# Kernel optimization log

Hardware: AMD Instinct MI355X
Metric: run time of the kernel (lower is better)

Reference implementation:

```python
import jax, jax.numpy as jnp
import numpy as np

T = 8192        # timesteps
IN = 512        # input_size
H = 1024        # hidden_layer_size
OUT = 256       # output_size
STEP = 0.25     # ODE solver step_size
NSUB = 4        # euler substeps per unit time interval (t spacing = 1)


def setup_inputs() -> dict:
    key = jax.random.key(0)
    ks = jax.random.split(key, 16)
    def lin(k, out_d, in_d):
        kw, kb = jax.random.split(k)
        W = jax.random.normal(kw, (out_d, in_d), jnp.float32) / np.sqrt(in_d).astype(np.float32)
        b = jax.random.normal(kb, (out_d, 1), jnp.float32) * 0.01
        return W, b
    W_in, b_in = lin(ks[0], H, IN)      # linear_in
    W_h, b_h = lin(ks[1], H, H)         # linear_hidden
    W_h2, b_h2 = lin(ks[2], H, H)       # linear_hidden2
    W_f1, b_f1 = lin(ks[3], H, H)       # ode_func.linear
    W_f2, b_f2 = lin(ks[4], H, H)       # ode_func.linear2
    W_dec, b_dec = lin(ks[5], OUT, H)   # decoder
    x = jax.random.normal(ks[6], (T, IN, 1), jnp.float32)
    t = jnp.arange(T, dtype=jnp.float32)
    return dict(t=t, x=x, W_in=W_in, b_in=b_in, W_h=W_h, b_h=b_h,
                W_h2=W_h2, b_h2=b_h2, W_f1=W_f1, b_f1=b_f1,
                W_f2=W_f2, b_f2=b_f2, W_dec=W_dec, b_dec=b_dec)


def reference(t, x, W_in, b_in, W_h, b_h, W_h2, b_h2, W_f1, b_f1, W_f2, b_f2, W_dec, b_dec):
    # ODE_Func: f(h) = W_f2 @ tanh(W_f1 @ h + b_f1) + b_f2   (autonomous; t unused)
    def ode_f(h):
        return W_f2 @ jnp.tanh(W_f1 @ h + b_f1) + b_f2

    dts = (t[1:] - t[:-1]) / NSUB  # (T-1,) euler substep sizes (fixed-grid euler)

    def step(h, inp):
        x_i, dt = inp
        # odeint(ode_func, h, t[i-1:i+1], method='euler', step_size=STEP)
        for _ in range(NSUB):
            h = h + dt * ode_f(h)
        # RNN cell update
        pre = W_in @ x_i + b_in + W_h @ h + b_h          # (H,1)
        h_new = jnp.tanh(W_h2 @ jnp.tanh(pre) + b_h2)    # (H,1)
        return h_new, None

    h0 = jnp.zeros((W_h.shape[0], 1), x.dtype)
    # original loop skips i == 0 entirely (h stays zeros there)
    h_T, _ = jax.lax.scan(step, h0, (x[1:], dts))
    return W_dec @ h_T + b_dec  # (OUT, 1)
```

## Files before the change

kernel.cpp:

```cpp
#include <hip/hip_runtime.h>
#include <math.h>


#define TSTEPS 8192
#define INP    512
#define HDIM   1024
#define OUTD   256
#define NWG    64
#define BLK    256
#define NREP   8

typedef unsigned long long u64;
typedef unsigned int u32;

__device__ __forceinline__ u64 aload(u64* p) {
    return __hip_atomic_load(p, __ATOMIC_RELAXED, __HIP_MEMORY_SCOPE_AGENT);
}
__device__ __forceinline__ void astore(u64* p, u64 v) {
    __hip_atomic_store(p, v, __ATOMIC_RELAXED, __HIP_MEMORY_SCOPE_AGENT);
}
__device__ __forceinline__ u64 pack(u32 tag, float f) {
    return ((u64)tag << 32) | (u64)__float_as_uint(f);
}

__global__ __launch_bounds__(256)
void mm1024(const float* __restrict__ A, const float* __restrict__ B,
            float* __restrict__ C) {
    __shared__ float As[64][17];
    __shared__ float Bs[16][65];
    const int tid = threadIdx.x;
    const int tx = tid & 15, ty = tid >> 4;
    const int r0 = blockIdx.y * 64, c0 = blockIdx.x * 64;
    float acc[4][4] = {};
    for (int k0 = 0; k0 < HDIM; k0 += 16) {
        const int ar = tid >> 2, ac = (tid & 3) * 4;
        const float4 av = *reinterpret_cast<const float4*>(
            A + (size_t)(r0 + ar) * HDIM + k0 + ac);
        As[ar][ac] = av.x; As[ar][ac + 1] = av.y;
        As[ar][ac + 2] = av.z; As[ar][ac + 3] = av.w;
        const int br = tid >> 4, bc = (tid & 15) * 4;
        const float4 bv = *reinterpret_cast<const float4*>(
            B + (size_t)(k0 + br) * HDIM + c0 + bc);
        Bs[br][bc] = bv.x; Bs[br][bc + 1] = bv.y;
        Bs[br][bc + 2] = bv.z; Bs[br][bc + 3] = bv.w;
        __syncthreads();
        #pragma unroll
        for (int kk = 0; kk < 16; ++kk) {
            float a[4], b[4];
            #pragma unroll
            for (int i2 = 0; i2 < 4; ++i2) a[i2] = As[ty * 4 + i2][kk];
            #pragma unroll
            for (int j2 = 0; j2 < 4; ++j2) b[j2] = Bs[kk][tx * 4 + j2];
            #pragma unroll
            for (int i2 = 0; i2 < 4; ++i2)
                #pragma unroll
                for (int j2 = 0; j2 < 4; ++j2)
                    acc[i2][j2] = fmaf(a[i2], b[j2], acc[i2][j2]);
        }
        __syncthreads();
    }
    #pragma unroll
    for (int i2 = 0; i2 < 4; ++i2)
        #pragma unroll
        for (int j2 = 0; j2 < 4; ++j2)
            C[(size_t)(r0 + ty * 4 + i2) * HDIM + c0 + tx * 4 + j2] = acc[i2][j2];
}

__global__ __launch_bounds__(BLK, 1)
void ode_rnn_persistent(
    const float* __restrict__ t,    const float* __restrict__ x,
    const float* __restrict__ W_in, const float* __restrict__ b_in,
    const float* __restrict__ W_h,  const float* __restrict__ b_h,
    const float* __restrict__ W_h2, const float* __restrict__ b_h2,
    const float* __restrict__ W_f1, const float* __restrict__ b_f1,
    const float* __restrict__ b_f2,
    const float* __restrict__ W_dec, const float* __restrict__ b_dec,
    const float* __restrict__ Mw,   const float* __restrict__ Pw,
    float* __restrict__ out,
    u64* QA, u64* QB, u64* QC, u64* QD)
{
    __shared__ __align__(16) float lds[HDIM];
    const int tid = threadIdx.x;
    const int wg  = blockIdx.x;
    const int seg = tid & 15;
    const int row = wg * 16 + (tid >> 4);
    const int rep = wg & (NREP - 1);

    auto publish = [&](u64* q, u32 e, float pre) {
        if (seg < 8) astore(q + (size_t)seg * HDIM + row, pack(e, tanhf(pre)));
    };

    auto stage = [&](u64* q, u32 tag) {
        u64* base = q + (size_t)rep * HDIM;
        __syncthreads();
        const int i0 = tid, i1 = tid + 256, i2 = tid + 512, i3 = tid + 768;
        u64 v0, v1, v2, v3;
        for (;;) {
            v0 = aload(base + i0); v1 = aload(base + i1);
            v2 = aload(base + i2); v3 = aload(base + i3);
            const bool ok = ((u32)(v0 >> 32) == tag) & ((u32)(v1 >> 32) == tag) &
                            ((u32)(v2 >> 32) == tag) & ((u32)(v3 >> 32) == tag);
            if (ok) break;
        }
        lds[i0] = __uint_as_float((u32)v0); lds[i1] = __uint_as_float((u32)v1);
        lds[i2] = __uint_as_float((u32)v2); lds[i3] = __uint_as_float((u32)v3);
        __syncthreads();
    };

    auto pref16 = [&](const float* W, float4 (&w)[16]) {
        const float4* pW = reinterpret_cast<const float4*>(W + (size_t)row * HDIM);
        #pragma unroll
        for (int j = 0; j < 16; ++j) w[j] = pW[j * 16 + seg];
    };
    auto red16 = [&](float a) {
        #pragma unroll
        for (int off = 8; off; off >>= 1) a += __shfl_xor(a, off, 16);
        return a;
    };
    auto dotLds = [&](const float4 (&w)[16]) {
        float a = 0.f;
        #pragma unroll
        for (int j = 0; j < 16; ++j) {
            const float4 v = *reinterpret_cast<const float4*>(lds + j * 64 + seg * 4);
            a = fmaf(w[j].x, v.x, a); a = fmaf(w[j].y, v.y, a);
            a = fmaf(w[j].z, v.z, a); a = fmaf(w[j].w, v.w, a);
        }
        return red16(a);
    };
    auto dotLds2 = [&](const float4 (&wa)[16], const float4 (&wb)[16],
                       float& oa, float& ob) {
        float a = 0.f, b = 0.f;
        #pragma unroll
        for (int j = 0; j < 16; ++j) {
            const float4 v = *reinterpret_cast<const float4*>(lds + j * 64 + seg * 4);
            a = fmaf(wa[j].x, v.x, a); a = fmaf(wa[j].y, v.y, a);
            a = fmaf(wa[j].z, v.z, a); a = fmaf(wa[j].w, v.w, a);
            b = fmaf(wb[j].x, v.x, b); b = fmaf(wb[j].y, v.y, b);
            b = fmaf(wb[j].z, v.z, b); b = fmaf(wb[j].w, v.w, b);
        }
        oa = red16(a); ob = red16(b);
    };

    float4 m16[16], p16[16], wir[8];
    pref16(Mw, m16);
    pref16(Pw, p16);
    {
        const float4* pW = reinterpret_cast<const float4*>(W_in + (size_t)row * INP);
        #pragma unroll
        for (int j = 0; j < 8; ++j) wir[j] = pW[j * 16 + seg];
    }

    const float bf1_r = b_f1[row];
    const float bih_r = b_in[row] + b_h[row];
    const float bh2_r = b_h2[row];

    float4 wbufA[16], wbufB[16];

    float c1_own, c2_own;
    {
        #pragma unroll
        for (int k = 0; k < 4; ++k) lds[tid + k * 256] = b_f2[tid + k * 256];
        __syncthreads();
        pref16(W_f1, wbufA); c1_own = dotLds(wbufA);
        pref16(W_h,  wbufA); c2_own = dotLds(wbufA);
    }

    float z_own = bf1_r;
    float y_own = 0.f;
    u32 eA = 0, eB = 0, eC = 0, eD = 0;
    float4 xr[8];

    #pragma unroll 1
    for (int i = 1; i < TSTEPS; ++i) {
        const float dt = (t[i] - t[i - 1]) * 0.25f;

        ++eA;
        publish(QA, eA, z_own);
        stage(QA, eA);
        {
            const float4* xp = reinterpret_cast<const float4*>(x + (size_t)i * INP);
            #pragma unroll
            for (int j = 0; j < 8; ++j) xr[j] = xp[j * 16 + seg];
        }
        {
            float md, pd; dotLds2(m16, p16, md, pd);
            z_own = fmaf(dt, md + c1_own, z_own);
            y_own = fmaf(dt, pd + c2_own, y_own);
        }

        ++eB;
        publish(QB, eB, z_own);
        stage(QB, eB);
        {
            float md, pd; dotLds2(m16, p16, md, pd);
            z_own = fmaf(dt, md + c1_own, z_own);
            y_own = fmaf(dt, pd + c2_own, y_own);
        }

        ++eA;
        publish(QA, eA, z_own);
        stage(QA, eA);
        {
            float md, pd; dotLds2(m16, p16, md, pd);
            z_own = fmaf(dt, md + c1_own, z_own);
            y_own = fmaf(dt, pd + c2_own, y_own);
        }

        ++eB;
        publish(QB, eB, z_own);
        float winx;
        {
            float a = 0.f;
            #pragma unroll
            for (int j = 0; j < 8; ++j) {
                a = fmaf(wir[j].x, xr[j].x, a); a = fmaf(wir[j].y, xr[j].y, a);
                a = fmaf(wir[j].z, xr[j].z, a); a = fmaf(wir[j].w, xr[j].w, a);
            }
            winx = red16(a);
        }
        stage(QB, eB);
        pref16(W_h2, wbufA);
        float apre;
        {
            const float pd = dotLds(p16);
            apre = fmaf(dt, pd + c2_own, y_own) + winx + bih_r;
        }

        ++eC;
        publish(QC, eC, apre);
        stage(QC, eC);
        pref16(W_f1, wbufB);
        const float hpre = dotLds(wbufA) + bh2_r;

        ++eD;
        publish(QD, eD, hpre);
        pref16(W_h, wbufA);
        stage(QD, eD);
        {
            float zd, yd; dotLds2(wbufB, wbufA, zd, yd);
            z_own = zd + bf1_r;
            y_own = yd;
        }
    }

    {
        const int rl = tid >> 6, s2 = tid & 63;
        const int orow = wg * 4 + rl;
        const float4* wd = reinterpret_cast<const float4*>(W_dec + (size_t)orow * HDIM);
        float acc = 0.f;
        #pragma unroll
        for (int j = 0; j < 4; ++j) {
            const float4 w = wd[j * 64 + s2];
            const float4 v = *reinterpret_cast<const float4*>(lds + j * 256 + s2 * 4);
            acc = fmaf(w.x, v.x, acc); acc = fmaf(w.y, v.y, acc);
            acc = fmaf(w.z, v.z, acc); acc = fmaf(w.w, v.w, acc);
        }
        #pragma unroll
        for (int off = 32; off; off >>= 1) acc += __shfl_down(acc, off, 64);
        if (s2 == 0) out[orow] = acc + b_dec[orow];
    }
}

extern "C" void kernel_launch(void* const* d_in, const int* in_sizes, int n_in,
                              void* d_out, int out_size, void* d_ws, size_t ws_size,
                              hipStream_t stream) {
    const float* t     = (const float*)d_in[0];
    const float* x     = (const float*)d_in[1];
    const float* W_in  = (const float*)d_in[2];
    const float* b_in  = (const float*)d_in[3];
    const float* W_h   = (const float*)d_in[4];
    const float* b_h   = (const float*)d_in[5];
    const float* W_h2  = (const float*)d_in[6];
    const float* b_h2  = (const float*)d_in[7];
    const float* W_f1  = (const float*)d_in[8];
    const float* b_f1  = (const float*)d_in[9];
    const float* W_f2  = (const float*)d_in[10];
    const float* b_f2  = (const float*)d_in[11];
    const float* W_dec = (const float*)d_in[12];
    const float* b_dec = (const float*)d_in[13];
    float* out = (float*)d_out;

    unsigned char* ws = (unsigned char*)d_ws;
    float* Mw = (float*)(ws);
    float* Pw = (float*)(ws + (size_t)4 * 1024 * 1024);
    u64*   QA = (u64*)(ws + (size_t)8 * 1024 * 1024);
    u64*   QB = QA + (size_t)NREP * HDIM;
    u64*   QC = QB + (size_t)NREP * HDIM;
    u64*   QD = QC + (size_t)NREP * HDIM;

    mm1024<<<dim3(16, 16), 256, 0, stream>>>(W_f1, W_f2, Mw);
    mm1024<<<dim3(16, 16), 256, 0, stream>>>(W_h,  W_f2, Pw);

    hipMemsetAsync(ws + (size_t)8 * 1024 * 1024, 0,
                   (size_t)4 * NREP * HDIM * sizeof(u64), stream);

    ode_rnn_persistent<<<dim3(NWG), dim3(BLK), 0, stream>>>(
        t, x, W_in, b_in, W_h, b_h, W_h2, b_h2, W_f1, b_f1, b_f2,
        W_dec, b_dec, Mw, Pw, out, QA, QB, QC, QD);
}
```

Baseline: 105.3 ms.

## Cache W_f1/W_h2 in LDS, accumulate state sum, and triple-buffer staging

Each workgroup now keeps its 16 rows of W_h2 and W_f1 in 144KB of dynamic LDS and W_h in registers, so weights are no longer re-fetched from global memory every timestep. The W_h·h term is no longer carried through the Euler substeps. It is rebuilt by accumulating the broadcast tanh vectors in LDS and applying Pw once per step, with W_h·h_prev computed while waiting on the next exchange. Triple-buffered staging with wave-level __all polling replaces the per-stage leading __syncthreads. The 8 replicated publish queues become a single queue. The aim is to cut global traffic and barrier latency on the serial critical path. The risks are more contention on the one queue and heavy LDS use.

```diff
diff --git a/kernel.cpp b/kernel.cpp
--- a/kernel.cpp
+++ b/kernel.cpp
@@ -5,10 +5,8 @@
 #define TSTEPS 8192
 #define INP    512
 #define HDIM   1024
-#define OUTD   256
 #define NWG    64
 #define BLK    256
-#define NREP   8
 
 typedef unsigned long long u64;
 typedef unsigned int u32;
@@ -79,135 +77,148 @@
     float* __restrict__ out,
     u64* QA, u64* QB, u64* QC, u64* QD)
 {
-    __shared__ __align__(16) float lds[HDIM];
-    const int tid = threadIdx.x;
-    const int wg  = blockIdx.x;
-    const int seg = tid & 15;
-    const int row = wg * 16 + (tid >> 4);
-    const int rep = wg & (NREP - 1);
-
-    auto publish = [&](u64* q, u32 e, float pre) {
-        if (seg < 8) astore(q + (size_t)seg * HDIM + row, pack(e, tanhf(pre)));
-    };
-
-    auto stage = [&](u64* q, u32 tag) {
-        u64* base = q + (size_t)rep * HDIM;
-        __syncthreads();
-        const int i0 = tid, i1 = tid + 256, i2 = tid + 512, i3 = tid + 768;
-        u64 v0, v1, v2, v3;
-        for (;;) {
-            v0 = aload(base + i0); v1 = aload(base + i1);
-            v2 = aload(base + i2); v3 = aload(base + i3);
-            const bool ok = ((u32)(v0 >> 32) == tag) & ((u32)(v1 >> 32) == tag) &
-                            ((u32)(v2 >> 32) == tag) & ((u32)(v3 >> 32) == tag);
-            if (ok) break;
-        }
-        lds[i0] = __uint_as_float((u32)v0); lds[i1] = __uint_as_float((u32)v1);
-        lds[i2] = __uint_as_float((u32)v2); lds[i3] = __uint_as_float((u32)v3);
-        __syncthreads();
-    };
-
-    auto pref16 = [&](const float* W, float4 (&w)[16]) {
-        const float4* pW = reinterpret_cast<const float4*>(W + (size_t)row * HDIM);
-        #pragma unroll
-        for (int j = 0; j < 16; ++j) w[j] = pW[j * 16 + seg];
-    };
-    auto red16 = [&](float a) {
-        #pragma unroll
-        for (int off = 8; off; off >>= 1) a += __shfl_xor(a, off, 16);
-        return a;
-    };
-    auto dotLds = [&](const float4 (&w)[16]) {
-        float a = 0.f;
+    extern __shared__ float smem[];
+    float* wh2l = smem;
+    float* wf1l = smem + 16 * 1024;
+    float* sb0  = smem + 32 * 1024;
+    float* sb1  = sb0 + 1024;
+    float* sb2  = sb1 + 1024;
+    float* us   = sb2 + 1024;
+
+    const int tid  = threadIdx.x;
+    const int wg   = blockIdx.x;
+    const int seg  = tid & 15;
+    const int rloc = tid >> 4;
+    const int row  = wg * 16 + rloc;
+
+    {
+        const float* s2 = W_h2 + (size_t)wg * 16 * HDIM;
+        const float* s1 = W_f1 + (size_t)wg * 16 * HDIM;
+        for (int k = 0; k < 16; ++k) {
+            const int idx = k * 1024 + tid * 4;
+            *reinterpret_cast<float4*>(wh2l + idx) =
+                *reinterpret_cast<const float4*>(s2 + idx);
+            *reinterpret_cast<float4*>(wf1l + idx) =
+                *reinterpret_cast<const float4*>(s1 + idx);
+        }
+    }
+
+    float4 m16[16], p16[16], whr[16], wir[8], xr[8];
+    {
+        const float4* pM = reinterpret_cast<const float4*>(Mw  + (size_t)row * HDIM);
+        const float4* pP = reinterpret_cast<const float4*>(Pw  + (size_t)row * HDIM);
+        const float4* pH = reinterpret_cast<const float4*>(W_h + (size_t)row * HDIM);
         #pragma unroll
         for (int j = 0; j < 16; ++j) {
-            const float4 v = *reinterpret_cast<const float4*>(lds + j * 64 + seg * 4);
-            a = fmaf(w[j].x, v.x, a); a = fmaf(w[j].y, v.y, a);
-            a = fmaf(w[j].z, v.z, a); a = fmaf(w[j].w, v.w, a);
-        }
-        return red16(a);
-    };
-    auto dotLds2 = [&](const float4 (&wa)[16], const float4 (&wb)[16],
-                       float& oa, float& ob) {
-        float a = 0.f, b = 0.f;
-        #pragma unroll
-        for (int j = 0; j < 16; ++j) {
-            const float4 v = *reinterpret_cast<const float4*>(lds + j * 64 + seg * 4);
-            a = fmaf(wa[j].x, v.x, a); a = fmaf(wa[j].y, v.y, a);
-            a = fmaf(wa[j].z, v.z, a); a = fmaf(wa[j].w, v.w, a);
-            b = fmaf(wb[j].x, v.x, b); b = fmaf(wb[j].y, v.y, b);
-            b = fmaf(wb[j].z, v.z, b); b = fmaf(wb[j].w, v.w, b);
-        }
-        oa = red16(a); ob = red16(b);
-    };
-
-    float4 m16[16], p16[16], wir[8];
-    pref16(Mw, m16);
-    pref16(Pw, p16);
-    {
-        const float4* pW = reinterpret_cast<const float4*>(W_in + (size_t)row * INP);
-        #pragma unroll
-        for (int j = 0; j < 8; ++j) wir[j] = pW[j * 16 + seg];
+            m16[j] = pM[j * 16 + seg];
+            p16[j] = pP[j * 16 + seg];
+            whr[j] = pH[j * 16 + seg];
+        }
+        const float4* pI = reinterpret_cast<const float4*>(W_in + (size_t)row * INP);
+        #pragma unroll
+        for (int j = 0; j < 8; ++j) wir[j] = pI[j * 16 + seg];
+        const float4* xp = reinterpret_cast<const float4*>(x + (size_t)1 * INP);
+        #pragma unroll
+        for (int j = 0; j < 8; ++j) xr[j] = xp[j * 16 + seg];
     }
 
     const float bf1_r = b_f1[row];
     const float bih_r = b_in[row] + b_h[row];
     const float bh2_r = b_h2[row];
 
-    float4 wbufA[16], wbufB[16];
-
-    float c1_own, c2_own;
-    {
-        #pragma unroll
-        for (int k = 0; k < 4; ++k) lds[tid + k * 256] = b_f2[tid + k * 256];
+    auto red16 = [&](float a) {
+        #pragma unroll
+        for (int off = 8; off; off >>= 1) a += __shfl_xor(a, off, 16);
+        return a;
+    };
+    auto dotReg = [&](const float4* w, const float* v) {
+        float a = 0.f;
+        #pragma unroll
+        for (int j = 0; j < 16; ++j) {
+            const float4 vv = *reinterpret_cast<const float4*>(v + j * 64 + seg * 4);
+            a = fmaf(w[j].x, vv.x, a); a = fmaf(w[j].y, vv.y, a);
+            a = fmaf(w[j].z, vv.z, a); a = fmaf(w[j].w, vv.w, a);
+        }
+        return red16(a);
+    };
+    auto dotW = [&](const float* Wl, const float* v) {
+        const float* wr = Wl + rloc * 1024;
+        float a = 0.f;
+        #pragma unroll
+        for (int j = 0; j < 16; ++j) {
+            const float4 w  = *reinterpret_cast<const float4*>(wr + j * 64 + seg * 4);
+            const float4 vv = *reinterpret_cast<const float4*>(v  + j * 64 + seg * 4);
+            a = fmaf(w.x, vv.x, a); a = fmaf(w.y, vv.y, a);
+            a = fmaf(w.z, vv.z, a); a = fmaf(w.w, vv.w, a);
+        }
+        return red16(a);
+    };
+    auto pub = [&](u64* q, u32 e, float pre) {
+        if (seg == 0) astore(&q[row], pack(e, tanhf(pre)));
+    };
+
+    int pb = 0;
+    auto stage = [&](u64* q, u32 tag, int mode) -> float* {
+        float* dst = (pb == 0) ? sb0 : (pb == 1) ? sb1 : sb2;
+        pb = (pb == 2) ? 0 : pb + 1;
+        const int i0 = tid, i1 = tid + 256, i2 = tid + 512, i3 = tid + 768;
+        u64 A0 = aload(q + i0), A1 = aload(q + i1), A2 = aload(q + i2), A3 = aload(q + i3);
+        u64 B0 = aload(q + i0), B1 = aload(q + i1), B2 = aload(q + i2), B3 = aload(q + i3);
+        u64 r0, r1, r2, r3;
+        for (;;) {
+            bool ok = ((u32)(A0 >> 32) == tag) & ((u32)(A1 >> 32) == tag) &
+                      ((u32)(A2 >> 32) == tag) & ((u32)(A3 >> 32) == tag);
+            if (__all(ok)) { r0 = A0; r1 = A1; r2 = A2; r3 = A3; break; }
+            A0 = aload(q + i0); A1 = aload(q + i1); A2 = aload(q + i2); A3 = aload(q + i3);
+            ok = ((u32)(B0 >> 32) == tag) & ((u32)(B1 >> 32) == tag) &
+                 ((u32)(B2 >> 32) == tag) & ((u32)(B3 >> 32) == tag);
+            if (__all(ok)) { r0 = B0; r1 = B1; r2 = B2; r3 = B3; break; }
+            B0 = aload(q + i0); B1 = aload(q + i1); B2 = aload(q + i2); B3 = aload(q + i3);
+        }
+        const float v0 = __uint_as_float((u32)r0), v1 = __uint_as_float((u32)r1);
+        const float v2 = __uint_as_float((u32)r2), v3 = __uint_as_float((u32)r3);
+        dst[i0] = v0; dst[i1] = v1; dst[i2] = v2; dst[i3] = v3;
+        if (mode == 1)      { us[i0]  = v0; us[i1]  = v1; us[i2]  = v2; us[i3]  = v3; }
+        else if (mode == 2) { us[i0] += v0; us[i1] += v1; us[i2] += v2; us[i3] += v3; }
         __syncthreads();
-        pref16(W_f1, wbufA); c1_own = dotLds(wbufA);
-        pref16(W_h,  wbufA); c2_own = dotLds(wbufA);
-    }
+        return dst;
+    };
+
+    __syncthreads();
+    #pragma unroll
+    for (int k = 0; k < 4; ++k) sb0[tid + k * 256] = b_f2[tid + k * 256];
+    __syncthreads();
+    const float c1_own = dotW(wf1l, sb0);
+    const float c2_own = dotReg(whr, sb0);
+    __syncthreads();
 
     float z_own = bf1_r;
-    float y_own = 0.f;
+    float yd_own = 0.f;
     u32 eA = 0, eB = 0, eC = 0, eD = 0;
-    float4 xr[8];
+    float* hprev = sb0;
 
     #pragma unroll 1
     for (int i = 1; i < TSTEPS; ++i) {
         const float dt = (t[i] - t[i - 1]) * 0.25f;
 
         ++eA;
-        publish(QA, eA, z_own);
-        stage(QA, eA);
-        {
-            const float4* xp = reinterpret_cast<const float4*>(x + (size_t)i * INP);
-            #pragma unroll
-            for (int j = 0; j < 8; ++j) xr[j] = xp[j * 16 + seg];
-        }
-        {
-            float md, pd; dotLds2(m16, p16, md, pd);
-            z_own = fmaf(dt, md + c1_own, z_own);
-            y_own = fmaf(dt, pd + c2_own, y_own);
-        }
+        pub(QA, eA, z_own);
+        float* b1 = stage(QA, eA, 1);
+        z_own = fmaf(dt, dotReg(m16, b1) + c1_own, z_own);
 
         ++eB;
-        publish(QB, eB, z_own);
-        stage(QB, eB);
-        {
-            float md, pd; dotLds2(m16, p16, md, pd);
-            z_own = fmaf(dt, md + c1_own, z_own);
-            y_own = fmaf(dt, pd + c2_own, y_own);
-        }
+        pub(QB, eB, z_own);
+        if (i > 1) yd_own = dotReg(whr, hprev);
+        float* b2 = stage(QB, eB, 2);
+        z_own = fmaf(dt, dotReg(m16, b2) + c1_own, z_own);
 
         ++eA;
-        publish(QA, eA, z_own);
-        stage(QA, eA);
-        {
-            float md, pd; dotLds2(m16, p16, md, pd);
-            z_own = fmaf(dt, md + c1_own, z_own);
-            y_own = fmaf(dt, pd + c2_own, y_own);
-        }
+        pub(QA, eA, z_own);
+        float* b3 = stage(QA, eA, 2);
+        z_own = fmaf(dt, dotReg(m16, b3) + c1_own, z_own);
 
         ++eB;
-        publish(QB, eB, z_own);
+        pub(QB, eB, z_own);
         float winx;
         {
             float a = 0.f;
@@ -218,29 +229,26 @@
             }
             winx = red16(a);
         }
-        stage(QB, eB);
-        pref16(W_h2, wbufA);
-        float apre;
+        stage(QB, eB, 2);
+        const float pd = dotReg(p16, us);
+        const float apre = fmaf(dt, pd + 4.f * c2_own, yd_own) + winx + bih_r;
+
+        ++eC;
+        pub(QC, eC, apre);
+        float* b5 = stage(QC, eC, 0);
+        const float hpre = dotW(wh2l, b5) + bh2_r;
+
+        ++eD;
+        pub(QD, eD, hpre);
         {
-            const float pd = dotLds(p16);
-            apre = fmaf(dt, pd + c2_own, y_own) + winx + bih_r;
-        }
-
-        ++eC;
-        publish(QC, eC, apre);
-        stage(QC, eC);
-        pref16(W_f1, wbufB);
-        const float hpre = dotLds(wbufA) + bh2_r;
-
-        ++eD;
-        publish(QD, eD, hpre);
-        pref16(W_h, wbufA);
-        stage(QD, eD);
-        {
-            float zd, yd; dotLds2(wbufB, wbufA, zd, yd);
-            z_own = zd + bf1_r;
-            y_own = yd;
-        }
+            const int inext = (i + 1 < TSTEPS) ? i + 1 : i;
+            const float4* xp = reinterpret_cast<const float4*>(x + (size_t)inext * INP);
+            #pragma unroll
+            for (int j = 0; j < 8; ++j) xr[j] = xp[j * 16 + seg];
+        }
+        float* b6 = stage(QD, eD, 0);
+        hprev = b6;
+        z_own = dotW(wf1l, b6) + bf1_r;
     }
 
     {
@@ -251,7 +259,7 @@
         #pragma unroll
         for (int j = 0; j < 4; ++j) {
             const float4 w = wd[j * 64 + s2];
-            const float4 v = *reinterpret_cast<const float4*>(lds + j * 256 + s2 * 4);
+            const float4 v = *reinterpret_cast<const float4*>(hprev + j * 256 + s2 * 4);
             acc = fmaf(w.x, v.x, acc); acc = fmaf(w.y, v.y, acc);
             acc = fmaf(w.z, v.z, acc); acc = fmaf(w.w, v.w, acc);
         }
@@ -284,17 +292,17 @@
     float* Mw = (float*)(ws);
     float* Pw = (float*)(ws + (size_t)4 * 1024 * 1024);
     u64*   QA = (u64*)(ws + (size_t)8 * 1024 * 1024);
-    u64*   QB = QA + (size_t)NREP * HDIM;
-    u64*   QC = QB + (size_t)NREP * HDIM;
-    u64*   QD = QC + (size_t)NREP * HDIM;
+    u64*   QB = QA + HDIM;
+    u64*   QC = QB + HDIM;
+    u64*   QD = QC + HDIM;
 
     mm1024<<<dim3(16, 16), 256, 0, stream>>>(W_f1, W_f2, Mw);
     mm1024<<<dim3(16, 16), 256, 0, stream>>>(W_h,  W_f2, Pw);
 
-    hipMemsetAsync(ws + (size_t)8 * 1024 * 1024, 0,
-                   (size_t)4 * NREP * HDIM * sizeof(u64), stream);
-
-    ode_rnn_persistent<<<dim3(NWG), dim3(BLK), 0, stream>>>(
+    hipMemsetAsync(ws + (size_t)8 * 1024 * 1024, 0, 4 * HDIM * sizeof(u64), stream);
+
+    const size_t smem_bytes = (size_t)(32 * 1024 + 4 * 1024) * sizeof(float);
+    ode_rnn_persistent<<<dim3(NWG), dim3(BLK), smem_bytes, stream>>>(
         t, x, W_in, b_in, W_h, b_h, W_h2, b_h2, W_f1, b_f1, b_f2,
         W_dec, b_dec, Mw, Pw, out, QA, QB, QC, QD);
 }
```

New measurement: 109.1 ms. 1.04x slower.
